# Performance work log

Hardware: AMD Instinct MI355X
Metric: run time of the kernel (lower is better)

Reference implementation:

```python
import jax, jax.numpy as jnp
import numpy as np

HEADS = 8
DIM_HEAD = 64
MAX_FREQ = 10.0


def _rope_tables(n):
    # RotaryEmbedding(dim_head//2): inv_freq over arange(0, 32, 2)/32 -> 16 freqs
    half = DIM_HEAD // 2  # 32
    inv_freq = 1.0 / (MAX_FREQ ** (jnp.arange(0, half, 2, dtype=jnp.float32) / half))  # [16]
    t = jnp.arange(n, dtype=jnp.float32)
    freqs = t[:, None] * inv_freq[None, :]          # [n, 16]
    freqs = jnp.concatenate([freqs, freqs], axis=-1)  # [n, 32]
    return jnp.cos(freqs), jnp.sin(freqs)


def _apply_rope(x, cos, sin):
    # x: [b, h, n, 64] split into pairs (d=32, r=2)
    b, h, n, dh = x.shape
    xr = x.reshape(b, h, n, dh // 2, 2)
    x1, x2 = xr[..., 0], xr[..., 1]                 # [b, h, n, 32]
    o1 = x1 * cos - x2 * sin                        # cos/sin: [n, 32] broadcast
    o2 = x1 * sin + x2 * cos
    return jnp.stack([o1, o2], axis=-1).reshape(b, h, n, dh)


def setup_inputs() -> dict:
    key = jax.random.key(0)
    k1, k2, k3, k4, k5, k6 = jax.random.split(key, 6)
    b, n, d = 2, 4096, 512
    inner = HEADS * DIM_HEAD  # 512
    s = lambda fan_in: 1.0 / np.sqrt(fan_in)
    return {
        "x": jax.random.normal(k1, (b, n, d), dtype=jnp.float32),
        "w_qkv": jax.random.normal(k2, (d, 3 * inner), dtype=jnp.float32) * s(d),
        "w_gates": jax.random.normal(k3, (d, HEADS), dtype=jnp.float32) * s(d),
        "b_gates": jax.random.normal(k4, (HEADS,), dtype=jnp.float32) * s(d),
        "w_out": jax.random.normal(k5, (inner, d), dtype=jnp.float32) * s(inner),
        "b_out": jax.random.normal(k6, (d,), dtype=jnp.float32) * s(inner),
    }


def reference(x, w_qkv, w_gates, b_gates, w_out, b_out):
    b, n, d = x.shape
    h, dh = HEADS, DIM_HEAD
    scale = dh ** -0.5

    qkv = x @ w_qkv                                  # [b, n, 3*h*dh]
    q, k, v = jnp.split(qkv, 3, axis=-1)
    to_bhnd = lambda t: t.reshape(b, n, h, dh).transpose(0, 2, 1, 3)
    q, k, v = to_bhnd(q), to_bhnd(k), to_bhnd(v)

    cos, sin = _rope_tables(n)
    q = _apply_rope(q, cos, sin)
    k = _apply_rope(k, cos, sin)

    dots = jnp.einsum('bhid,bhjd->bhij', q, k) * scale   # [b, h, n, n]
    attn = jax.nn.softmax(dots, axis=-1)

    gates = jax.nn.sigmoid(x @ w_gates + b_gates)        # [b, n, h]
    out = jnp.einsum('bhij,bhjd->bhid', attn, v)         # [b, h, n, dh]
    out = out * gates.transpose(0, 2, 1)[..., None]      # per-head sigmoid gate
    out = out.transpose(0, 2, 1, 3).reshape(b, n, h * dh)
    return out @ w_out + b_out
```

## Files before the change

### kernel.cpp

```cpp
#include <hip/hip_runtime.h>

typedef unsigned short u16;
typedef unsigned int u32;
typedef __attribute__((ext_vector_type(2))) unsigned int u32x2;
typedef __attribute__((ext_vector_type(4))) float f32x4;
typedef __attribute__((ext_vector_type(16))) float f32x16;
typedef __attribute__((ext_vector_type(8))) short s16x8;
typedef __attribute__((ext_vector_type(4))) short s16x4;

union U64 { u32 d[2]; s16x4 v; };
union U128 { u32 d[4]; s16x8 v; };

__device__ __forceinline__ u16 f2bf(float f) {
  u32 u = __builtin_bit_cast(u32, f);
  u += 0x7fffu + ((u >> 16) & 1u);
  return (u16)(u >> 16);
}

__device__ __forceinline__ u32 cvt_pk(float a, float b) {
  u32 r;
  asm("v_cvt_pk_bf16_f32 %0, %1, %2" : "=v"(r) : "v"(a), "v"(b));
  return r;
}

__device__ __forceinline__ void gload16(const void* g, void* l) {
  __builtin_amdgcn_global_load_lds((const __attribute__((address_space(1))) void*)g,
                                   (__attribute__((address_space(3))) void*)l, 16, 0, 0);
}

__global__ void rope_tab_kernel(float* __restrict__ ct, float* __restrict__ st) {
  int idx = blockIdx.x * 256 + threadIdx.x;
  int row = idx >> 5, col = idx & 31;
  int j = col & 15;
  float invf = __powf(10.0f, -(float)j * (1.0f / 16.0f));
  float ang = (float)row * invf;
  ct[idx] = cosf(ang);
  st[idx] = sinf(ang);
}

__global__ void convert_x_kernel(const float* __restrict__ x, u16* __restrict__ xb) {
  int i = blockIdx.x * 256 + threadIdx.x;
  f32x4 a = ((const f32x4*)x)[i * 2 + 0];
  f32x4 b = ((const f32x4*)x)[i * 2 + 1];
  s16x8 o;
  o[0] = (short)f2bf(a[0]); o[1] = (short)f2bf(a[1]);
  o[2] = (short)f2bf(a[2]); o[3] = (short)f2bf(a[3]);
  o[4] = (short)f2bf(b[0]); o[5] = (short)f2bf(b[1]);
  o[6] = (short)f2bf(b[2]); o[7] = (short)f2bf(b[3]);
  ((s16x8*)xb)[i] = o;
}

__global__ void transpose_conv_kernel(const float* __restrict__ in, u16* __restrict__ out,
                                      int R, int C) {
  __shared__ float tl[32][33];
  int c0 = blockIdx.x * 32, r0 = blockIdx.y * 32;
  int tx = threadIdx.x, ty = threadIdx.y;
#pragma unroll
  for (int i = 0; i < 4; i++)
    tl[ty + i * 8][tx] = in[(size_t)(r0 + ty + i * 8) * C + c0 + tx];
  __syncthreads();
#pragma unroll
  for (int i = 0; i < 4; i++)
    out[(size_t)(c0 + ty + i * 8) * R + r0 + tx] = f2bf(tl[tx][ty + i * 8]);
}

__global__ void gates_kernel(const float* __restrict__ x, const float* __restrict__ wg,
                             const float* __restrict__ bg, float* __restrict__ gates) {
  int t = threadIdx.x;
  int lane = t & 63, w = t >> 6;
  int row = blockIdx.x * 4 + w;
  float acc[8] = {0, 0, 0, 0, 0, 0, 0, 0};
#pragma unroll
  for (int kk = 0; kk < 8; kk++) {
    int k = kk * 64 + lane;
    float xv = x[(size_t)row * 512 + k];
    f32x4 w0 = ((const f32x4*)(wg + (size_t)k * 8))[0];
    f32x4 w1 = ((const f32x4*)(wg + (size_t)k * 8))[1];
    acc[0] += xv * w0[0]; acc[1] += xv * w0[1]; acc[2] += xv * w0[2]; acc[3] += xv * w0[3];
    acc[4] += xv * w1[0]; acc[5] += xv * w1[1]; acc[6] += xv * w1[2]; acc[7] += xv * w1[3];
  }
#pragma unroll
  for (int off = 32; off >= 1; off >>= 1) {
#pragma unroll
    for (int h = 0; h < 8; h++) acc[h] += __shfl_xor(acc[h], off);
  }
  if (lane < 8) {
    float v = acc[0];
#pragma unroll
    for (int hh = 1; hh < 8; hh++) if (lane == hh) v = acc[hh];
    v += bg[lane];
    gates[(size_t)row * 8 + lane] = 1.0f / (1.0f + __expf(-v));
  }
}

template <int EPI>
__global__ __launch_bounds__(256, 2) void gemm_kernel(
    const u16* __restrict__ A, const u16* __restrict__ Bt, float* __restrict__ outp, int Nc,
    const float* __restrict__ cost, const float* __restrict__ sint,
    const float* __restrict__ bias, u16* __restrict__ qkv, u16* __restrict__ vws) {
  __shared__ u16 Al[128][72];
  __shared__ u16 Bl[128][72];
  int t = threadIdx.x;
  int nb = Nc >> 7;
  int nwg = gridDim.x;
  int cpx = nwg >> 3;
  int swzb = (blockIdx.x & 7) * cpx + (blockIdx.x >> 3);
  int bm = swzb / nb, bn = swzb % nb;
  int m0 = bm << 7, n0 = bn << 7;
  int w = t >> 6, lane = t & 63, c = lane & 15, g = lane >> 4;
  int wr = w >> 1, wc = w & 1;
  f32x4 acc[4][4] = {};
  int ldr = t >> 3, ldj = t & 7;
  const u16* Ag = A + (size_t)m0 * 512;
  const u16* Bg = Bt + (size_t)n0 * 512;
  for (int k0 = 0; k0 < 512; k0 += 64) {
    __syncthreads();
#pragma unroll
    for (int rr = 0; rr < 4; rr++) {
      int row = ldr + rr * 32;
      *(s16x8*)&Al[row][ldj * 8] = *(const s16x8*)(Ag + (size_t)row * 512 + k0 + ldj * 8);
      *(s16x8*)&Bl[row][ldj * 8] = *(const s16x8*)(Bg + (size_t)row * 512 + k0 + ldj * 8);
    }
    __syncthreads();
#pragma unroll
    for (int ks = 0; ks < 2; ks++) {
      s16x8 af[4], bf[4];
#pragma unroll
      for (int mt = 0; mt < 4; mt++)
        af[mt] = *(const s16x8*)&Al[wr * 64 + mt * 16 + c][ks * 32 + g * 8];
#pragma unroll
      for (int nt = 0; nt < 4; nt++)
        bf[nt] = *(const s16x8*)&Bl[wc * 64 + nt * 16 + c][ks * 32 + g * 8];
#pragma unroll
      for (int mt = 0; mt < 4; mt++)
#pragma unroll
        for (int nt = 0; nt < 4; nt++)
          acc[mt][nt] = __builtin_amdgcn_mfma_f32_16x16x32_bf16(af[mt], bf[nt], acc[mt][nt], 0, 0, 0);
    }
  }
  if (EPI == 0) {
    int sect = n0 >> 9;
    if (sect < 2) {
#pragma unroll
      for (int mt = 0; mt < 4; mt++) {
#pragma unroll
        for (int nt = 0; nt < 4; nt++) {
#pragma unroll
          for (int r = 0; r < 4; r++) {
            int mrow = m0 + wr * 64 + mt * 16 + g * 4 + r;
            int cg = n0 + wc * 64 + nt * 16 + c;
            float val = acc[mt][nt][r];
            float other = __shfl_xor(val, 1);
            int p = (cg & 63) >> 1;
            int nidx = mrow & 4095;
            float cv = cost[nidx * 32 + p];
            float sv = sint[nidx * 32 + p];
            float o = (cg & 1) ? (other * sv + val * cv) : (val * cv - other * sv);
            if (sect == 0) o *= 0.18033688011f;
            qkv[(size_t)mrow * 1536 + cg] = f2bf(o);
          }
        }
      }
    } else {
#pragma unroll
      for (int mt = 0; mt < 4; mt++) {
#pragma unroll
        for (int nt = 0; nt < 4; nt++) {
          int cg = n0 + wc * 64 + nt * 16 + c;
          int vcol = cg - 1024;
          int hh = vcol >> 6, dh = vcol & 63;
          int mrowb = m0 + wr * 64 + mt * 16 + g * 4;
          int bb = mrowb >> 12, nn = mrowb & 4095;
          U64 u;
          u.d[0] = cvt_pk(acc[mt][nt][0], acc[mt][nt][1]);
          u.d[1] = cvt_pk(acc[mt][nt][2], acc[mt][nt][3]);
          *(s16x4*)(vws + ((size_t)(bb * 8 + hh) * 64 + dh) * 4096 + nn) = u.v;
        }
      }
    }
  } else {
#pragma unroll
    for (int mt = 0; mt < 4; mt++) {
#pragma unroll
      for (int nt = 0; nt < 4; nt++) {
#pragma unroll
        for (int r = 0; r < 4; r++) {
          int mrow = m0 + wr * 64 + mt * 16 + g * 4 + r;
          int cg = n0 + wc * 64 + nt * 16 + c;
          outp[(size_t)mrow * 512 + cg] = acc[mt][nt][r] + bias[cg];
        }
      }
    }
  }
}

__global__ __launch_bounds__(256, 3) void attn_kernel(const u16* __restrict__ qkv,
                                                      const u16* __restrict__ vT,
                                                      const float* __restrict__ gates,
                                                      u16* __restrict__ ao) {
  __shared__ u16 Kl[2][4096];
  __shared__ u16 Vl[2][4096];
  int t = threadIdx.x;
  int o = blockIdx.x;
  int bh = ((o & 7) << 1) + ((o >> 8) & 1);
  int qblk = (o >> 3) & 31;
  int b = bh >> 3, h = bh & 7;
  int w = t >> 6, lane = t & 63;
  int c32 = lane & 31, hi = lane >> 5;
  int q0 = qblk * 128 + w * 32;

  const char* qb = (const char*)qkv;
  const char* vb = (const char*)vT;
  u32 D0 = (u32)(w * 2048 + lane * 16);
  u32 D1 = D0 + 1024;
  u32 u0 = D0 ^ (((D0 >> 7) & 7) << 4);
  u32 u1 = D1 ^ (((D1 >> 7) & 7) << 4);
  const char* ksrc0 = qb + ((size_t)(b * 4096 + (D0 >> 7)) * 1536 + 512 + h * 64) * 2 + (u0 & 127);
  const char* ksrc1 = qb + ((size_t)(b * 4096 + (D1 >> 7)) * 1536 + 512 + h * 64) * 2 + (u1 & 127);
  const char* vsrc0 = vb + ((size_t)((b * 8 + h) * 64 + (D0 >> 7)) * 4096) * 2 + (u0 & 127);
  const char* vsrc1 = vb + ((size_t)((b * 8 + h) * 64 + (D1 >> 7)) * 4096) * 2 + (u1 & 127);

  s16x8 qf[4];
  {
    const u16* qp = qkv + (size_t)(b * 4096 + q0 + c32) * 1536 + h * 64 + hi * 8;
#pragma unroll
    for (int ks = 0; ks < 4; ks++) qf[ks] = *(const s16x8*)(qp + ks * 16);
  }

  s16x8 ones;
#pragma unroll
  for (int i = 0; i < 8; i++) ones[i] = (short)0x3f80;

  u32 rsw = (u32)((c32 & 7) << 4);
  const char* klb = (const char*)&Kl[0][0] + c32 * 128;
  const char* vlb = (const char*)&Vl[0][0] + c32 * 128;

  f32x16 acco[2] = {};
  f32x16 accl = {};

  {
    char* kd = (char*)&Kl[0][0] + w * 2048;
    char* vd = (char*)&Vl[0][0] + w * 2048;
    gload16(ksrc0, kd);
    gload16(ksrc1, kd + 1024);
    gload16(vsrc0, vd);
    gload16(vsrc1, vd + 1024);
  }
  __syncthreads();

  int cur = 0;
  for (int tile = 0; tile < 64; ++tile) {
    if (tile < 63) {
      int nbuf = cur ^ 1;
      size_t ka = (size_t)(tile + 1) * 196608;
      size_t va = (size_t)(tile + 1) * 128;
      char* kd = (char*)&Kl[0][0] + nbuf * 8192 + w * 2048;
      char* vd = (char*)&Vl[0][0] + nbuf * 8192 + w * 2048;
      gload16(ksrc0 + ka, kd);
      gload16(ksrc1 + ka, kd + 1024);
      gload16(vsrc0 + va, vd);
      gload16(vsrc1 + va, vd + 1024);
    }

    const char* kl = klb + cur * 8192;
    f32x16 sc[2] = {};
    __builtin_amdgcn_s_setprio(1);
#pragma unroll
    for (int kb = 0; kb < 2; kb++) {
#pragma unroll
      for (int ks = 0; ks < 4; ks++) {
        s16x8 kf = *(const s16x8*)(kl + kb * 4096 + (((u32)(ks * 32 + hi * 16)) ^ rsw));
        sc[kb] = __builtin_amdgcn_mfma_f32_32x32x16_bf16(kf, qf[ks], sc[kb], 0, 0, 0);
      }
    }
    __builtin_amdgcn_s_setprio(0);

#pragma unroll
    for (int kb = 0; kb < 2; kb++)
#pragma unroll
      for (int r = 0; r < 16; r++) sc[kb][r] = exp2f(sc[kb][r]);

    U128 pf[4];
#pragma unroll
    for (int kb = 0; kb < 2; kb++) {
#pragma unroll
      for (int s = 0; s < 2; s++) {
        u32 a1 = cvt_pk(sc[kb][s * 8 + 0], sc[kb][s * 8 + 1]);
        u32 b1 = cvt_pk(sc[kb][s * 8 + 4], sc[kb][s * 8 + 5]);
        u32 a2 = cvt_pk(sc[kb][s * 8 + 2], sc[kb][s * 8 + 3]);
        u32 b2 = cvt_pk(sc[kb][s * 8 + 6], sc[kb][s * 8 + 7]);
        u32x2 r1 = __builtin_amdgcn_permlane32_swap(a1, b1, false, false);
        u32x2 r2 = __builtin_amdgcn_permlane32_swap(a2, b2, false, false);
        pf[kb * 2 + s].d[0] = r1[0];
        pf[kb * 2 + s].d[1] = r2[0];
        pf[kb * 2 + s].d[2] = r1[1];
        pf[kb * 2 + s].d[3] = r2[1];
      }
    }

    const char* vl = vlb + cur * 8192;
    __builtin_amdgcn_s_setprio(1);
#pragma unroll
    for (int ks = 0; ks < 4; ks++) {
#pragma unroll
      for (int db = 0; db < 2; db++) {
        s16x8 vf = *(const s16x8*)(vl + db * 4096 + (((u32)(ks * 32 + hi * 16)) ^ rsw));
        acco[db] = __builtin_amdgcn_mfma_f32_32x32x16_bf16(vf, pf[ks].v, acco[db], 0, 0, 0);
      }
      accl = __builtin_amdgcn_mfma_f32_32x32x16_bf16(ones, pf[ks].v, accl, 0, 0, 0);
    }
    __builtin_amdgcn_s_setprio(0);

    __syncthreads();
    cur ^= 1;
  }

  float linv = 1.0f / accl[0];
  int row = b * 4096 + q0 + c32;
  float gr = gates[(size_t)row * 8 + h] * linv;
  u16* op = ao + (size_t)row * 512 + h * 64 + hi * 4;
#pragma unroll
  for (int db = 0; db < 2; db++)
#pragma unroll
    for (int grp = 0; grp < 4; grp++) {
      U64 u;
      u.d[0] = cvt_pk(acco[db][grp * 4 + 0] * gr, acco[db][grp * 4 + 1] * gr);
      u.d[1] = cvt_pk(acco[db][grp * 4 + 2] * gr, acco[db][grp * 4 + 3] * gr);
      *(s16x4*)(op + db * 32 + grp * 8) = u.v;
    }
}

extern "C" void kernel_launch(void* const* d_in, const int* in_sizes, int n_in,
                              void* d_out, int out_size, void* d_ws, size_t ws_size,
                              hipStream_t stream) {
  (void)in_sizes; (void)n_in; (void)out_size; (void)ws_size;
  const float* x = (const float*)d_in[0];
  const float* w_qkv = (const float*)d_in[1];
  const float* w_gates = (const float*)d_in[2];
  const float* b_gates = (const float*)d_in[3];
  const float* w_out = (const float*)d_in[4];
  const float* b_out = (const float*)d_in[5];
  float* out = (float*)d_out;

  char* ws = (char*)d_ws;
  size_t off = 0;
  u16* qkv_ws = (u16*)(ws + off); off += (size_t)2 * 4096 * 1536 * 2;
  u16* vws    = (u16*)(ws + off); off += (size_t)2 * 8 * 64 * 4096 * 2;
  u16* x_bf   = (u16*)(ws + off); off += (size_t)8192 * 512 * 2;
  u16* wqkvT  = (u16*)(ws + off); off += (size_t)1536 * 512 * 2;
  u16* woutT  = (u16*)(ws + off); off += (size_t)512 * 512 * 2;
  float* cost = (float*)(ws + off); off += (size_t)4096 * 32 * 4;
  float* sint = (float*)(ws + off); off += (size_t)4096 * 32 * 4;
  float* gts  = (float*)(ws + off); off += (size_t)8192 * 8 * 4;
  u16* attno  = (u16*)(ws + off); off += (size_t)8192 * 512 * 2;

  hipLaunchKernelGGL(rope_tab_kernel, dim3(512), dim3(256), 0, stream, cost, sint);
  hipLaunchKernelGGL(convert_x_kernel, dim3(2048), dim3(256), 0, stream, x, x_bf);
  hipLaunchKernelGGL(transpose_conv_kernel, dim3(48, 16), dim3(32, 8), 0, stream,
                     w_qkv, wqkvT, 512, 1536);
  hipLaunchKernelGGL(transpose_conv_kernel, dim3(16, 16), dim3(32, 8), 0, stream,
                     w_out, woutT, 512, 512);
  hipLaunchKernelGGL(gates_kernel, dim3(2048), dim3(256), 0, stream, x, w_gates, b_gates, gts);
  hipLaunchKernelGGL(gemm_kernel<0>, dim3((8192 / 128) * (1536 / 128)), dim3(256), 0, stream,
                     x_bf, wqkvT, nullptr, 1536, cost, sint, nullptr, qkv_ws, vws);
  hipLaunchKernelGGL(attn_kernel, dim3(512), dim3(256), 0, stream, qkv_ws, vws, gts, attno);
  hipLaunchKernelGGL(gemm_kernel<1>, dim3((8192 / 128) * (512 / 128)), dim3(256), 0, stream,
                     attno, woutT, out, 512, nullptr, nullptr, b_out, nullptr, nullptr);
}
```

Measured before the change: 256.3 us.

## Split attention KV range across two blocks and combine partials

Splits each attention query block's key/value sequence into two halves handled by separate workgroups, doubling the grid to 1024 blocks. Each block writes unnormalized fp32 partial outputs and row sums to workspace, and a new combine kernel adds them, applies the gate and normalization, and writes bf16. The aim is better CU occupancy on the 256-CU device, where 512 blocks under-fill it. The cost is extra global traffic for the fp32 partials (about 32MB written and read) plus an additional kernel launch. Launch bounds also change from 3 to 2 waves per SIMD. The exp has no max subtraction, so summing the partials without rescaling is consistent.

```diff
diff --git a/kernel.cpp b/kernel.cpp
--- a/kernel.cpp
+++ b/kernel.cpp
@@ -194,20 +194,24 @@
   }
 }
 
-__global__ __launch_bounds__(256, 3) void attn_kernel(const u16* __restrict__ qkv,
+__global__ __launch_bounds__(256, 2) void attn_kernel(const u16* __restrict__ qkv,
                                                       const u16* __restrict__ vT,
-                                                      const float* __restrict__ gates,
-                                                      u16* __restrict__ ao) {
+                                                      float* __restrict__ pO,
+                                                      float* __restrict__ pl) {
   __shared__ u16 Kl[2][4096];
   __shared__ u16 Vl[2][4096];
   int t = threadIdx.x;
   int o = blockIdx.x;
-  int bh = ((o & 7) << 1) + ((o >> 8) & 1);
-  int qblk = (o >> 3) & 31;
+  int j = o >> 3;
+  int bh = ((o & 7) << 1) + (j >> 6);
+  int rest = j & 63;
+  int qblk = rest >> 1;
+  int ks2 = rest & 1;
   int b = bh >> 3, h = bh & 7;
   int w = t >> 6, lane = t & 63;
   int c32 = lane & 31, hi = lane >> 5;
   int q0 = qblk * 128 + w * 32;
+  int kvbase = ks2 * 2048;
 
   const char* qb = (const char*)qkv;
   const char* vb = (const char*)vT;
@@ -215,10 +219,10 @@
   u32 D1 = D0 + 1024;
   u32 u0 = D0 ^ (((D0 >> 7) & 7) << 4);
   u32 u1 = D1 ^ (((D1 >> 7) & 7) << 4);
-  const char* ksrc0 = qb + ((size_t)(b * 4096 + (D0 >> 7)) * 1536 + 512 + h * 64) * 2 + (u0 & 127);
-  const char* ksrc1 = qb + ((size_t)(b * 4096 + (D1 >> 7)) * 1536 + 512 + h * 64) * 2 + (u1 & 127);
-  const char* vsrc0 = vb + ((size_t)((b * 8 + h) * 64 + (D0 >> 7)) * 4096) * 2 + (u0 & 127);
-  const char* vsrc1 = vb + ((size_t)((b * 8 + h) * 64 + (D1 >> 7)) * 4096) * 2 + (u1 & 127);
+  const char* ksrc0 = qb + ((size_t)(b * 4096 + kvbase + (D0 >> 7)) * 1536 + 512 + h * 64) * 2 + (u0 & 127);
+  const char* ksrc1 = qb + ((size_t)(b * 4096 + kvbase + (D1 >> 7)) * 1536 + 512 + h * 64) * 2 + (u1 & 127);
+  const char* vsrc0 = vb + ((size_t)((b * 8 + h) * 64 + (D0 >> 7)) * 4096 + kvbase) * 2 + (u0 & 127);
+  const char* vsrc1 = vb + ((size_t)((b * 8 + h) * 64 + (D1 >> 7)) * 4096 + kvbase) * 2 + (u1 & 127);
 
   s16x8 qf[4];
   {
@@ -249,8 +253,8 @@
   __syncthreads();
 
   int cur = 0;
-  for (int tile = 0; tile < 64; ++tile) {
-    if (tile < 63) {
+  for (int tile = 0; tile < 32; ++tile) {
+    if (tile < 31) {
       int nbuf = cur ^ 1;
       size_t ka = (size_t)(tile + 1) * 196608;
       size_t va = (size_t)(tile + 1) * 128;
@@ -284,17 +288,17 @@
 #pragma unroll
     for (int kb = 0; kb < 2; kb++) {
 #pragma unroll
-      for (int s = 0; s < 2; s++) {
-        u32 a1 = cvt_pk(sc[kb][s * 8 + 0], sc[kb][s * 8 + 1]);
-        u32 b1 = cvt_pk(sc[kb][s * 8 + 4], sc[kb][s * 8 + 5]);
-        u32 a2 = cvt_pk(sc[kb][s * 8 + 2], sc[kb][s * 8 + 3]);
-        u32 b2 = cvt_pk(sc[kb][s * 8 + 6], sc[kb][s * 8 + 7]);
+      for (int ss = 0; ss < 2; ss++) {
+        u32 a1 = cvt_pk(sc[kb][ss * 8 + 0], sc[kb][ss * 8 + 1]);
+        u32 b1 = cvt_pk(sc[kb][ss * 8 + 4], sc[kb][ss * 8 + 5]);
+        u32 a2 = cvt_pk(sc[kb][ss * 8 + 2], sc[kb][ss * 8 + 3]);
+        u32 b2 = cvt_pk(sc[kb][ss * 8 + 6], sc[kb][ss * 8 + 7]);
         u32x2 r1 = __builtin_amdgcn_permlane32_swap(a1, b1, false, false);
         u32x2 r2 = __builtin_amdgcn_permlane32_swap(a2, b2, false, false);
-        pf[kb * 2 + s].d[0] = r1[0];
-        pf[kb * 2 + s].d[1] = r2[0];
-        pf[kb * 2 + s].d[2] = r1[1];
-        pf[kb * 2 + s].d[3] = r2[1];
+        pf[kb * 2 + ss].d[0] = r1[0];
+        pf[kb * 2 + ss].d[1] = r2[0];
+        pf[kb * 2 + ss].d[2] = r1[1];
+        pf[kb * 2 + ss].d[3] = r2[1];
       }
     }
 
@@ -315,19 +319,38 @@
     cur ^= 1;
   }
 
-  float linv = 1.0f / accl[0];
-  int row = b * 4096 + q0 + c32;
-  float gr = gates[(size_t)row * 8 + h] * linv;
-  u16* op = ao + (size_t)row * 512 + h * 64 + hi * 4;
+  size_t prow = ((size_t)(bh * 32 + qblk) * 2 + ks2) * 128 + w * 32 + c32;
+  float* po = pO + prow * 64 + hi * 4;
 #pragma unroll
   for (int db = 0; db < 2; db++)
 #pragma unroll
     for (int grp = 0; grp < 4; grp++) {
-      U64 u;
-      u.d[0] = cvt_pk(acco[db][grp * 4 + 0] * gr, acco[db][grp * 4 + 1] * gr);
-      u.d[1] = cvt_pk(acco[db][grp * 4 + 2] * gr, acco[db][grp * 4 + 3] * gr);
-      *(s16x4*)(op + db * 32 + grp * 8) = u.v;
-    }
+      f32x4 v;
+      v[0] = acco[db][grp * 4 + 0]; v[1] = acco[db][grp * 4 + 1];
+      v[2] = acco[db][grp * 4 + 2]; v[3] = acco[db][grp * 4 + 3];
+      *(f32x4*)(po + db * 32 + grp * 8) = v;
+    }
+  if (hi == 0) pl[prow] = accl[0];
+}
+
+__global__ void combine_kernel(const float* __restrict__ pO, const float* __restrict__ pl,
+                               const float* __restrict__ gates, u16* __restrict__ ao) {
+  int idx = blockIdx.x * 256 + threadIdx.x;
+  int rowg = idx >> 4;
+  int dq = (idx & 15) * 4;
+  int bh = rowg >> 12, q = rowg & 4095;
+  int qblk = q >> 7, rb = q & 127;
+  size_t pr0 = ((size_t)(bh * 32 + qblk) * 2 + 0) * 128 + rb;
+  size_t pr1 = pr0 + 128;
+  float l = pl[pr0] + pl[pr1];
+  f32x4 a = *(const f32x4*)(pO + pr0 * 64 + dq);
+  f32x4 c = *(const f32x4*)(pO + pr1 * 64 + dq);
+  int b = bh >> 3, h = bh & 7;
+  float g = gates[((size_t)(b * 4096 + q)) * 8 + h] / l;
+  U64 u;
+  u.d[0] = cvt_pk((a[0] + c[0]) * g, (a[1] + c[1]) * g);
+  u.d[1] = cvt_pk((a[2] + c[2]) * g, (a[3] + c[3]) * g);
+  *(s16x4*)(ao + ((size_t)(b * 4096 + q)) * 512 + h * 64 + dq) = u.v;
 }
 
 extern "C" void kernel_launch(void* const* d_in, const int* in_sizes, int n_in,
@@ -353,6 +376,8 @@
   float* sint = (float*)(ws + off); off += (size_t)4096 * 32 * 4;
   float* gts  = (float*)(ws + off); off += (size_t)8192 * 8 * 4;
   u16* attno  = (u16*)(ws + off); off += (size_t)8192 * 512 * 2;
+  float* pO   = (float*)(ws + off); off += (size_t)131072 * 64 * 4;
+  float* pl   = (float*)(ws + off); off += (size_t)131072 * 4;
 
   hipLaunchKernelGGL(rope_tab_kernel, dim3(512), dim3(256), 0, stream, cost, sint);
   hipLaunchKernelGGL(convert_x_kernel, dim3(2048), dim3(256), 0, stream, x, x_bf);
@@ -363,7 +388,8 @@
   hipLaunchKernelGGL(gates_kernel, dim3(2048), dim3(256), 0, stream, x, w_gates, b_gates, gts);
   hipLaunchKernelGGL(gemm_kernel<0>, dim3((8192 / 128) * (1536 / 128)), dim3(256), 0, stream,
                      x_bf, wqkvT, nullptr, 1536, cost, sint, nullptr, qkv_ws, vws);
-  hipLaunchKernelGGL(attn_kernel, dim3(512), dim3(256), 0, stream, qkv_ws, vws, gts, attno);
+  hipLaunchKernelGGL(attn_kernel, dim3(1024), dim3(256), 0, stream, qkv_ws, vws, pO, pl);
+  hipLaunchKernelGGL(combine_kernel, dim3(4096), dim3(256), 0, stream, pO, pl, gts, attno);
   hipLaunchKernelGGL(gemm_kernel<1>, dim3((8192 / 128) * (512 / 128)), dim3(256), 0, stream,
                      attno, woutT, out, 512, nullptr, nullptr, b_out, nullptr, nullptr);
 }
```

Result: slower. 266.5 us (+4.0%).
